# Kernel tuning notes

Measured on AMD Instinct MI355X. Metric: run time of the kernel, lower is better.

## Reference

```python
import jax, jax.numpy as jnp
import numpy as np

DIM, HEADS, WIN, SHIFT = 384, 12, 7, 3
H, W = 56, 56
HEAD_DIM = DIM // HEADS
SCALE = HEAD_DIM ** -0.5
N = WIN * WIN


def _relative_index():
    coords = np.stack(np.meshgrid(np.arange(WIN), np.arange(WIN), indexing='ij')).reshape(2, -1)
    rel = (coords[:, :, None] - coords[:, None, :]).transpose(1, 2, 0)
    rel[:, :, 0] += WIN - 1
    rel[:, :, 1] += WIN - 1
    rel[:, :, 0] *= 2 * WIN - 1
    return rel.sum(-1)  # [N, N] int


def _attn_mask():
    img = np.zeros((H, W), dtype=np.float32)
    cnt = 0
    sls = (slice(0, -WIN), slice(-WIN, -SHIFT), slice(-SHIFT, None))
    for hs in sls:
        for ws in sls:
            img[hs, ws] = cnt
            cnt += 1
    m = img.reshape(H // WIN, WIN, W // WIN, WIN).transpose(0, 2, 1, 3).reshape(-1, N)  # [nw, N]
    diff = m[:, None, :] - m[:, :, None]  # [nw, N, N]
    return np.where(diff != 0, -10000.0, 0.0).astype(np.float32)

REL_IDX = jnp.asarray(_relative_index())
MASK = jnp.asarray(_attn_mask())  # [nw, N, N]


def _layernorm(x, w, b):
    mu = x.mean(-1, keepdims=True)
    var = ((x - mu) ** 2).mean(-1, keepdims=True)
    return (x - mu) * jax.lax.rsqrt(var + 1e-5) * w + b


def _window_partition(x):  # [B,H,W,C] -> [B*nw, N, C]
    B, _, _, C = x.shape
    x = x.reshape(B, H // WIN, WIN, W // WIN, WIN, C)
    x = x.transpose(0, 1, 3, 2, 4, 5)
    return x.reshape(-1, N, C)


def _window_reverse(w, B):  # [B*nw, N, C] -> [B,H,W,C]
    C = w.shape[-1]
    x = w.reshape(B, H // WIN, W // WIN, WIN, WIN, C)
    x = x.transpose(0, 1, 3, 2, 4, 5)
    return x.reshape(B, H, W, C)


def setup_inputs() -> dict:
    key = jax.random.key(0)
    ks = jax.random.split(key, 12)
    s = DIM ** -0.5
    return {
        'x': jax.random.normal(ks[0], (32, H * W, DIM), jnp.float32),
        'qkv_w': jax.random.normal(ks[1], (DIM, 3 * DIM), jnp.float32) * s,  # stored [in,out]
        'qkv_b': jnp.zeros((3 * DIM,), jnp.float32),
        'proj_w': jax.random.normal(ks[2], (DIM, DIM), jnp.float32) * s,
        'proj_b': jnp.zeros((DIM,), jnp.float32),
        'rel_bias': jax.random.normal(ks[3], ((2 * WIN - 1) ** 2, HEADS), jnp.float32) * 0.02,
        'norm1_w': jnp.ones((DIM,), jnp.float32),
        'norm1_b': jnp.zeros((DIM,), jnp.float32),
        'norm2_w': jnp.ones((DIM,), jnp.float32),
        'norm2_b': jnp.zeros((DIM,), jnp.float32),
        'mlp_w1': jax.random.normal(ks[4], (DIM, 4 * DIM), jnp.float32) * s,
        'mlp_b1': jnp.zeros((4 * DIM,), jnp.float32),
        'mlp_w2': jax.random.normal(ks[5], (4 * DIM, DIM), jnp.float32) * (4 * DIM) ** -0.5,
        'mlp_b2': jnp.zeros((DIM,), jnp.float32),
    }


def _forward(x, qkv_w, qkv_b, proj_w, proj_b, rel_bias, norm1_w, norm1_b,
             norm2_w, norm2_b, mlp_w1, mlp_b1, mlp_w2, mlp_b2):
    B, L, C = x.shape
    residual = x
    h = _layernorm(x, norm1_w, norm1_b).reshape(B, H, W, C)
    h = jnp.roll(h, (-SHIFT, -SHIFT), axis=(1, 2))
    wx = _window_partition(h)  # [B_, N, C]
    B_ = wx.shape[0]

    qkv = (wx @ qkv_w + qkv_b).reshape(B_, N, 3, HEADS, HEAD_DIM)
    q, k, v = qkv[:, :, 0], qkv[:, :, 1], qkv[:, :, 2]  # [B_, N, h, d]
    attn = jnp.einsum('bnhd,bmhd->bhnm', q * SCALE, k)  # [B_, h, N, N]
    rb = rel_bias[REL_IDX.reshape(-1)].reshape(N, N, HEADS).transpose(2, 0, 1)
    attn = attn + rb[None]
    nw = MASK.shape[0]
    attn = attn.reshape(B_ // nw, nw, HEADS, N, N) + MASK[None, :, None]
    attn = jax.nn.softmax(attn.reshape(B_, HEADS, N, N), axis=-1)
    out = jnp.einsum('bhnm,bmhd->bnhd', attn, v).reshape(B_, N, C)
    out = out @ proj_w + proj_b

    h = _window_reverse(out, B)
    h = jnp.roll(h, (SHIFT, SHIFT), axis=(1, 2))
    x = h.reshape(B, L, C) + residual

    m = _layernorm(x, norm2_w, norm2_b)
    m = jax.nn.gelu(m @ mlp_w1 + mlp_b1, approximate=False) @ mlp_w2 + mlp_b2
    return x + m


def reference(x, qkv_w, qkv_b, proj_w, proj_b, rel_bias, norm1_w, norm1_b,
              norm2_w, norm2_b, mlp_w1, mlp_b1, mlp_w2, mlp_b2):
    return _forward(x, qkv_w, qkv_b, proj_w, proj_b, rel_bias, norm1_w, norm1_b,
                    norm2_w, norm2_b, mlp_w1, mlp_b1, mlp_w2, mlp_b2)
```

## Files before the change

kernel.cpp:

```cpp
#include <hip/hip_runtime.h>
#include <hip/hip_bf16.h>

typedef unsigned short u16;
typedef __bf16 bf16x8 __attribute__((ext_vector_type(8)));
typedef float f32x4 __attribute__((ext_vector_type(4)));

#define HH 56
#define WW 56
#define DIM 384
#define NTOK 100352
#define NWIN 2048
#define NN 49

__device__ __forceinline__ u16 f2bf(float f) {
    __hip_bfloat16 h = __float2bfloat16(f);
    return *reinterpret_cast<u16*>(&h);
}
__device__ __forceinline__ float bf2f(u16 u) {
    union { unsigned int i; float f; } c; c.i = ((unsigned int)u) << 16; return c.f;
}

__device__ __forceinline__ float fast_gelu(float x) {
    float au = fabsf(x) * 0.70710678118654752f;
    float t = __builtin_amdgcn_rcpf(fmaf(0.3275911f, au, 1.0f));
    float p = fmaf(t, 1.061405429f, -1.453152027f);
    p = fmaf(t, p, 1.421413741f);
    p = fmaf(t, p, -0.284496736f);
    p = fmaf(t, p, 0.254829592f);
    p = p * t;
    float e = __expf(-au * au);
    float erfau = fmaf(-p, e, 1.0f);
    float erfx = __builtin_copysignf(erfau, x);
    return 0.5f * x * (1.0f + erfx);
}

#define GLD_LDS(gp, lp) __builtin_amdgcn_global_load_lds( \
    (const __attribute__((address_space(1))) void*)(gp), \
    (__attribute__((address_space(3))) void*)(lp), 16, 0, 0)

__global__ void castT(const float* __restrict__ in, u16* __restrict__ out, int K, int N) {
    int i = blockIdx.x * 256 + threadIdx.x;
    if (i < N * K) {
        int n = i / K, kk = i - n * K;
        out[i] = f2bf(in[(size_t)kk * N + n]);
    }
}

__global__ void bias_kernel(const float* __restrict__ rel_bias, float* __restrict__ Tb) {
    int ty = blockIdx.x / 12, h = blockIdx.x - ty * 12;
    for (int i = threadIdx.x; i < 4096; i += 256) {
        int q = i >> 6, kk = i & 63;
        float v;
        if (kk >= 49) v = -1e30f;
        else if (q >= 49) v = 0.f;
        else {
            int rn = q / 7, cn = q - rn * 7;
            int rm = kk / 7, cm = kk - rm * 7;
            float rb = rel_bias[((rn - rm + 6) * 13 + (cn - cm + 6)) * 12 + h];
            int h0 = (ty >> 1) ? 49 : 0;
            int w0 = (ty & 1) ? 49 : 0;
            int hn = h0 + rn, hm = h0 + rm, wn = w0 + cn, wm = w0 + cm;
            int regn = (hn < 49 ? 0 : (hn < 53 ? 1 : 2)) * 3 + (wn < 49 ? 0 : (wn < 53 ? 1 : 2));
            int regm = (hm < 49 ? 0 : (hm < 53 ? 1 : 2)) * 3 + (wm < 49 ? 0 : (wm < 53 ? 1 : 2));
            v = rb + ((regn == regm) ? 0.f : -10000.f);
        }
        Tb[(size_t)blockIdx.x * 4096 + i] = v;
    }
}

template<bool WIN_MAP>
__global__ __launch_bounds__(256) void ln_kernel(
    const float* __restrict__ x, const float* __restrict__ w, const float* __restrict__ b,
    u16* __restrict__ out)
{
    int token = blockIdx.x * 4 + (threadIdx.x >> 6);
    int lane = threadIdx.x & 63;
    const float* row = x + (size_t)token * DIM;
    float v[6]; float sum = 0.f, sq = 0.f;
#pragma unroll
    for (int j = 0; j < 3; j++) {
        float2 p = *(const float2*)(row + lane * 2 + j * 128);
        v[2*j] = p.x; v[2*j+1] = p.y;
        sum += p.x + p.y; sq += p.x * p.x + p.y * p.y;
    }
#pragma unroll
    for (int off = 32; off; off >>= 1) { sum += __shfl_xor(sum, off); sq += __shfl_xor(sq, off); }
    float mu = sum * (1.f / DIM);
    float rstd = rsqrtf(sq * (1.f / DIM) - mu * mu + 1e-5f);
    size_t obase;
    if (WIN_MAP) {
        int b_ = token / 3136, hw = token - b_ * 3136;
        int h = hw / WW, wc_ = hw - h * WW;
        int hr = h - 3; if (hr < 0) hr += HH;
        int wr = wc_ - 3; if (wr < 0) wr += WW;
        int win = b_ * 64 + (hr / 7) * 8 + (wr / 7);
        int n = (hr % 7) * 7 + (wr % 7);
        obase = ((size_t)win * NN + n) * DIM;
    } else {
        obase = (size_t)token * DIM;
    }
#pragma unroll
    for (int j = 0; j < 3; j++) {
        int c = lane * 2 + j * 128;
        float a0 = (v[2*j]   - mu) * rstd * w[c]   + b[c];
        float a1 = (v[2*j+1] - mu) * rstd * w[c+1] + b[c+1];
        unsigned int pair = (unsigned int)f2bf(a0) | ((unsigned int)f2bf(a1) << 16);
        *(unsigned int*)(out + obase + c) = pair;
    }
}

template<int EPI>
__global__ __launch_bounds__(256, 3) void gemm_kernel(
    const u16* __restrict__ A, const u16* __restrict__ Bt,
    const float* __restrict__ bias, const float* __restrict__ resid,
    void* __restrict__ outp, int N, int K, int BNT)
{
    __shared__ u16 sA[3][4096];
    __shared__ u16 sB[3][4096];
    const int tid = threadIdx.x;
    const int lane = tid & 63;
    const int wave = tid >> 6;
    const int wr = wave >> 1, wc = wave & 1;

    const int q8 = gridDim.x >> 3;
    const int wg = (blockIdx.x & 7) * q8 + (blockIdx.x >> 3);
    const int bm = wg / BNT, bn = wg - bm * BNT;

    f32x4 acc[4][4] = {};

    const int r0 = tid >> 2;
    const int sg = (tid & 3) ^ (r0 & 3) ^ ((r0 >> 2) & 3);
    const u16* Arow0 = A + (size_t)(bm * 128 + r0) * K + sg * 8;
    const u16* Arow1 = Arow0 + (size_t)64 * K;
    const u16* Brow0 = Bt + (size_t)(bn * 128 + r0) * K + sg * 8;
    const u16* Brow1 = Brow0 + (size_t)64 * K;

    const int nt = K >> 5;

#define STAGE(t, buf) do { \
        int kt_ = (t) * 32; \
        GLD_LDS(Arow0 + kt_, &sA[buf][wave * 512]); \
        GLD_LDS(Arow1 + kt_, &sA[buf][2048 + wave * 512]); \
        GLD_LDS(Brow0 + kt_, &sB[buf][wave * 512]); \
        GLD_LDS(Brow1 + kt_, &sB[buf][2048 + wave * 512]); \
    } while (0)

    STAGE(0, 0); STAGE(1, 1);

    const int l15 = lane & 15, g = lane >> 4;
    const int ssr = (g ^ (l15 & 3) ^ ((l15 >> 2) & 3)) * 8;

    int buf = 0;
    for (int t = 0; t < nt; t++) {
        if (EPI == 3) {
            __builtin_amdgcn_s_barrier();
            __builtin_amdgcn_sched_barrier(0);
            if (t + 2 < nt) {
                int nb = buf + 2; if (nb >= 3) nb -= 3;
                STAGE(t + 2, nb);
            }
            int rem = nt - 1 - t; if (rem > 2) rem = 2;
            if (rem == 2)      asm volatile("s_waitcnt vmcnt(8)" ::: "memory");
            else if (rem == 1) asm volatile("s_waitcnt vmcnt(4)" ::: "memory");
            else               asm volatile("s_waitcnt vmcnt(0)" ::: "memory");
            __builtin_amdgcn_s_barrier();
            __builtin_amdgcn_sched_barrier(0);
        } else {
            if (t + 1 < nt) asm volatile("s_waitcnt vmcnt(4)" ::: "memory");
            else            asm volatile("s_waitcnt vmcnt(0)" ::: "memory");
            __builtin_amdgcn_s_barrier();
            __builtin_amdgcn_sched_barrier(0);
            if (t + 2 < nt) {
                int nb = buf + 2; if (nb >= 3) nb -= 3;
                STAGE(t + 2, nb);
            }
        }
        bf16x8 af[4], bfr[4];
#pragma unroll
        for (int m = 0; m < 4; m++) {
            int row = wr * 64 + m * 16 + l15;
            af[m] = *(const bf16x8*)&sA[buf][row * 32 + ssr];
        }
#pragma unroll
        for (int n = 0; n < 4; n++) {
            int row = wc * 64 + n * 16 + l15;
            bfr[n] = *(const bf16x8*)&sB[buf][row * 32 + ssr];
        }
#pragma unroll
        for (int m = 0; m < 4; m++)
#pragma unroll
            for (int n = 0; n < 4; n++)
                acc[m][n] = __builtin_amdgcn_mfma_f32_16x16x32_bf16(af[m], bfr[n], acc[m][n], 0, 0, 0);
        buf = buf + 1; if (buf >= 3) buf = 0;
    }
#undef STAGE

    const int col0 = bn * 128 + wc * 64 + l15;
    float bias4[4];
#pragma unroll
    for (int nn = 0; nn < 4; nn++) bias4[nn] = bias[col0 + nn * 16];

#pragma unroll
    for (int m = 0; m < 4; m++) {
#pragma unroll
        for (int r = 0; r < 4; r++) {
            int row = bm * 128 + wr * 64 + m * 16 + (g << 2) + r;
            size_t obase;
            if (EPI == 1) {
                int win = row / NN, n = row - win * NN;
                int b_ = win >> 6, wi = win & 63;
                int hr = (wi >> 3) * 7 + n / 7;
                int wcl = (wi & 7) * 7 + n % 7;
                int hf = hr + 3; if (hf >= HH) hf -= HH;
                int wf = wcl + 3; if (wf >= WW) wf -= WW;
                obase = ((size_t)b_ * 3136 + hf * WW + wf) * DIM;
            } else {
                obase = (size_t)row * N;
            }
#pragma unroll
            for (int nn = 0; nn < 4; nn++) {
                int col = col0 + nn * 16;
                float val = acc[m][nn][r] + bias4[nn];
                if (EPI == 0) {
                    ((u16*)outp)[obase + col] = f2bf(val);
                } else if (EPI == 1) {
                    ((float*)outp)[obase + col] = val + resid[obase + col];
                } else if (EPI == 2) {
                    ((u16*)outp)[obase + col] = f2bf(fast_gelu(val));
                } else {
                    ((float*)outp)[obase + col] = val + resid[obase + col];
                }
            }
        }
    }
}

__global__ __launch_bounds__(256) void attn_kernel(
    const u16* __restrict__ qkv, const float* __restrict__ Tb,
    u16* __restrict__ attn_out)
{
    __shared__ u16 smem[4][6912];
    const int win = blockIdx.x;
    const int wave = threadIdx.x >> 6;
    const int lane = threadIdx.x & 63;
    const int head = blockIdx.y * 4 + wave;
    const int l15 = lane & 15, g = lane >> 4;

    u16* Vt = smem[wave];
    u16* P  = Vt + 2304;

    const u16* qkvw = qkv + (size_t)win * NN * 1152 + head * 32;

    {
        int m = lane;
        bool real = m < NN;
        const u16* vrow = qkvw + (size_t)(real ? m : 0) * 1152 + 768;
        int4 z = {0,0,0,0};
        int4 c0 = real ? *(const int4*)(vrow)      : z;
        int4 c1 = real ? *(const int4*)(vrow + 8)  : z;
        int4 c2 = real ? *(const int4*)(vrow + 16) : z;
        int4 c3 = real ? *(const int4*)(vrow + 24) : z;
        u16 vals[32];
        *(int4*)&vals[0]  = c0; *(int4*)&vals[8]  = c1;
        *(int4*)&vals[16] = c2; *(int4*)&vals[24] = c3;
#pragma unroll
        for (int d = 0; d < 32; d++) Vt[d * 72 + m] = vals[d];
    }

    bf16x8 kf[4], qf[4];
#pragma unroll
    for (int t = 0; t < 4; t++) {
        int row = t * 16 + l15; if (row > 48) row = 48;
        const u16* base = qkvw + (size_t)row * 1152 + g * 8;
        kf[t] = *(const bf16x8*)(base + 384);
        qf[t] = *(const bf16x8*)(base);
    }
    f32x4 s[4][4];
#pragma unroll
    for (int mt = 0; mt < 4; mt++)
#pragma unroll
        for (int nt = 0; nt < 4; nt++) {
            f32x4 zero = {};
            s[mt][nt] = __builtin_amdgcn_mfma_f32_16x16x32_bf16(kf[mt], qf[nt], zero, 0, 0, 0);
        }

    const int wi = win & 63;
    const int ty = (((wi >> 3) == 7) ? 2 : 0) + (((wi & 7) == 7) ? 1 : 0);
    const float* tbb = Tb + (((size_t)ty * 12 + head) << 12);
    const float SCALE = 0.17677669529663687f;
#pragma unroll
    for (int nt = 0; nt < 4; nt++) {
        int q = nt * 16 + l15;
        const float* trow = tbb + q * 64 + g * 4;
        f32x4 b[4];
#pragma unroll
        for (int mt = 0; mt < 4; mt++) b[mt] = *(const f32x4*)(trow + mt * 16);
        float mx = -3e38f;
#pragma unroll
        for (int mt = 0; mt < 4; mt++)
#pragma unroll
            for (int r = 0; r < 4; r++) {
                float v = s[mt][nt][r] * SCALE + b[mt][r];
                s[mt][nt][r] = v;
                mx = fmaxf(mx, v);
            }
        mx = fmaxf(mx, __shfl_xor(mx, 16));
        mx = fmaxf(mx, __shfl_xor(mx, 32));
        float sum = 0.f;
#pragma unroll
        for (int mt = 0; mt < 4; mt++)
#pragma unroll
            for (int r = 0; r < 4; r++) {
                float e = __expf(s[mt][nt][r] - mx);
                s[mt][nt][r] = e;
                sum += e;
            }
        sum += __shfl_xor(sum, 16);
        sum += __shfl_xor(sum, 32);
        float inv = 1.f / sum;
#pragma unroll
        for (int mt = 0; mt < 4; mt++) {
            unsigned int p01 = (unsigned int)f2bf(s[mt][nt][0] * inv) | ((unsigned int)f2bf(s[mt][nt][1] * inv) << 16);
            unsigned int p23 = (unsigned int)f2bf(s[mt][nt][2] * inv) | ((unsigned int)f2bf(s[mt][nt][3] * inv) << 16);
            uint2 pk; pk.x = p01; pk.y = p23;
            *(uint2*)&P[(unsigned)q * 72 + mt * 16 + g * 4] = pk;
        }
    }

    bf16x8 vf[2][2];
#pragma unroll
    for (int ks = 0; ks < 2; ks++)
#pragma unroll
        for (int dt = 0; dt < 2; dt++)
            vf[ks][dt] = *(const bf16x8*)&Vt[(dt * 16 + l15) * 72 + ks * 32 + g * 8];

    f32x4 o[4][2] = {};
#pragma unroll
    for (int nt = 0; nt < 4; nt++) {
        bf16x8 pf0 = *(const bf16x8*)&P[(nt * 16 + l15) * 72 + g * 8];
        bf16x8 pf1 = *(const bf16x8*)&P[(nt * 16 + l15) * 72 + 32 + g * 8];
#pragma unroll
        for (int dt = 0; dt < 2; dt++) {
            o[nt][dt] = __builtin_amdgcn_mfma_f32_16x16x32_bf16(pf0, vf[0][dt], o[nt][dt], 0, 0, 0);
            o[nt][dt] = __builtin_amdgcn_mfma_f32_16x16x32_bf16(pf1, vf[1][dt], o[nt][dt], 0, 0, 0);
        }
    }

#pragma unroll
    for (int nt = 0; nt < 4; nt++)
#pragma unroll
        for (int r = 0; r < 4; r++) {
            int q = nt * 16 + 4 * g + r;
            if (q < NN) {
                size_t ob = ((size_t)win * NN + q) * DIM + head * 32;
                attn_out[ob + l15]      = f2bf(o[nt][0][r]);
                attn_out[ob + 16 + l15] = f2bf(o[nt][1][r]);
            }
        }
}

extern "C" void kernel_launch(void* const* d_in, const int* in_sizes, int n_in,
                              void* d_out, int out_size, void* d_ws, size_t ws_size,
                              hipStream_t stream)
{
    const float* x      = (const float*)d_in[0];
    const float* qkv_w  = (const float*)d_in[1];
    const float* qkv_b  = (const float*)d_in[2];
    const float* proj_w = (const float*)d_in[3];
    const float* proj_b = (const float*)d_in[4];
    const float* rel_b  = (const float*)d_in[5];
    const float* n1w    = (const float*)d_in[6];
    const float* n1b    = (const float*)d_in[7];
    const float* n2w    = (const float*)d_in[8];
    const float* n2b    = (const float*)d_in[9];
    const float* w1     = (const float*)d_in[10];
    const float* b1     = (const float*)d_in[11];
    const float* w2     = (const float*)d_in[12];
    const float* b2     = (const float*)d_in[13];

    char* ws = (char*)d_ws;
    u16* hidden  = (u16*)(ws);
    u16* qkvbuf  = hidden;
    float* Tb    = (float*)(ws + 231211008);
    u16* wxbuf   = (u16*)(ws + 308281344);
    u16* qkv_wt  = (u16*)(ws + 385351680);
    u16* proj_wt = (u16*)(ws + 386236416);
    u16* w1t     = (u16*)(ws + 386531328);
    u16* w2t     = (u16*)(ws + 387710976);

    castT<<<(1152*384 + 255) / 256, 256, 0, stream>>>(qkv_w, qkv_wt, 384, 1152);
    castT<<<(384*384  + 255) / 256, 256, 0, stream>>>(proj_w, proj_wt, 384, 384);
    castT<<<(384*1536 + 255) / 256, 256, 0, stream>>>(w1, w1t, 384, 1536);
    castT<<<(1536*384 + 255) / 256, 256, 0, stream>>>(w2, w2t, 1536, 384);
    bias_kernel<<<48, 256, 0, stream>>>(rel_b, Tb);

    ln_kernel<true><<<NTOK / 4, 256, 0, stream>>>(x, n1w, n1b, wxbuf);
    gemm_kernel<0><<<784 * 9, 256, 0, stream>>>(wxbuf, qkv_wt, qkv_b, nullptr, qkvbuf, 1152, 384, 9);
    attn_kernel<<<dim3(NWIN, 3), 256, 0, stream>>>(qkvbuf, Tb, wxbuf);
    gemm_kernel<1><<<784 * 3, 256, 0, stream>>>(wxbuf, proj_wt, proj_b, x, d_out, 384, 384, 3);
    ln_kernel<false><<<NTOK / 4, 256, 0, stream>>>((const float*)d_out, n2w, n2b, wxbuf);
    gemm_kernel<2><<<784 * 12, 256, 0, stream>>>(wxbuf, w1t, b1, nullptr, hidden, 1536, 384, 12);
    gemm_kernel<3><<<784 * 3, 256, 0, stream>>>(hidden, w2t, b2, (const float*)d_out, d_out, 384, 1536, 3);
}
```

Before: 929.4 us.

## Fuse window attention, output projection, residual and LayerNorm2 into one kernel

The attention kernel now handles all 12 heads of a window in one block. It keeps the per-head outputs in a swizzled LDS tile, runs the 384x384 projection GEMM directly from LDS, adds bias and the residual, writes y1, and computes LayerNorm2 statistics through LDS atomics before writing the bf16 normalized output. This removes the separate proj GEMM launch, the standalone LN2 kernel, and the round trips of the attention output and y1 through global memory. In exchange, each block uses about 80 KB of LDS, which lowers occupancy. The projection weight fragments are read straight from global memory with no LDS staging, and the special wait schedule for the EPI==3 GEMM variant is removed.

New measurement: 991.4 us. 1.07x slower.

```diff
diff --git a/kernel.cpp b/kernel.cpp
--- a/kernel.cpp
+++ b/kernel.cpp
@@ -68,7 +68,6 @@
     }
 }
 
-template<bool WIN_MAP>
 __global__ __launch_bounds__(256) void ln_kernel(
     const float* __restrict__ x, const float* __restrict__ w, const float* __restrict__ b,
     u16* __restrict__ out)
@@ -87,18 +86,13 @@
     for (int off = 32; off; off >>= 1) { sum += __shfl_xor(sum, off); sq += __shfl_xor(sq, off); }
     float mu = sum * (1.f / DIM);
     float rstd = rsqrtf(sq * (1.f / DIM) - mu * mu + 1e-5f);
-    size_t obase;
-    if (WIN_MAP) {
-        int b_ = token / 3136, hw = token - b_ * 3136;
-        int h = hw / WW, wc_ = hw - h * WW;
-        int hr = h - 3; if (hr < 0) hr += HH;
-        int wr = wc_ - 3; if (wr < 0) wr += WW;
-        int win = b_ * 64 + (hr / 7) * 8 + (wr / 7);
-        int n = (hr % 7) * 7 + (wr % 7);
-        obase = ((size_t)win * NN + n) * DIM;
-    } else {
-        obase = (size_t)token * DIM;
-    }
+    int b_ = token / 3136, hw = token - b_ * 3136;
+    int h = hw / WW, wc_ = hw - h * WW;
+    int hr = h - 3; if (hr < 0) hr += HH;
+    int wr = wc_ - 3; if (wr < 0) wr += WW;
+    int win = b_ * 64 + (hr / 7) * 8 + (wr / 7);
+    int n = (hr % 7) * 7 + (wr % 7);
+    size_t obase = ((size_t)win * NN + n) * DIM;
 #pragma unroll
     for (int j = 0; j < 3; j++) {
         int c = lane * 2 + j * 128;
@@ -152,28 +146,13 @@
 
     int buf = 0;
     for (int t = 0; t < nt; t++) {
-        if (EPI == 3) {
-            __builtin_amdgcn_s_barrier();
-            __builtin_amdgcn_sched_barrier(0);
-            if (t + 2 < nt) {
-                int nb = buf + 2; if (nb >= 3) nb -= 3;
-                STAGE(t + 2, nb);
-            }
-            int rem = nt - 1 - t; if (rem > 2) rem = 2;
-            if (rem == 2)      asm volatile("s_waitcnt vmcnt(8)" ::: "memory");
-            else if (rem == 1) asm volatile("s_waitcnt vmcnt(4)" ::: "memory");
-            else               asm volatile("s_waitcnt vmcnt(0)" ::: "memory");
-            __builtin_amdgcn_s_barrier();
-            __builtin_amdgcn_sched_barrier(0);
-        } else {
-            if (t + 1 < nt) asm volatile("s_waitcnt vmcnt(4)" ::: "memory");
-            else            asm volatile("s_waitcnt vmcnt(0)" ::: "memory");
-            __builtin_amdgcn_s_barrier();
-            __builtin_amdgcn_sched_barrier(0);
-            if (t + 2 < nt) {
-                int nb = buf + 2; if (nb >= 3) nb -= 3;
-                STAGE(t + 2, nb);
-            }
+        if (t + 1 < nt) asm volatile("s_waitcnt vmcnt(4)" ::: "memory");
+        else            asm volatile("s_waitcnt vmcnt(0)" ::: "memory");
+        __builtin_amdgcn_s_barrier();
+        __builtin_amdgcn_sched_barrier(0);
+        if (t + 2 < nt) {
+            int nb = buf + 2; if (nb >= 3) nb -= 3;
+            STAGE(t + 2, nb);
         }
         bf16x8 af[4], bfr[4];
 #pragma unroll
@@ -205,26 +184,13 @@
 #pragma unroll
         for (int r = 0; r < 4; r++) {
             int row = bm * 128 + wr * 64 + m * 16 + (g << 2) + r;
-            size_t obase;
-            if (EPI == 1) {
-                int win = row / NN, n = row - win * NN;
-                int b_ = win >> 6, wi = win & 63;
-                int hr = (wi >> 3) * 7 + n / 7;
-                int wcl = (wi & 7) * 7 + n % 7;
-                int hf = hr + 3; if (hf >= HH) hf -= HH;
-                int wf = wcl + 3; if (wf >= WW) wf -= WW;
-                obase = ((size_t)b_ * 3136 + hf * WW + wf) * DIM;
-            } else {
-                obase = (size_t)row * N;
-            }
+            size_t obase = (size_t)row * N;
 #pragma unroll
             for (int nn = 0; nn < 4; nn++) {
                 int col = col0 + nn * 16;
                 float val = acc[m][nn][r] + bias4[nn];
                 if (EPI == 0) {
                     ((u16*)outp)[obase + col] = f2bf(val);
-                } else if (EPI == 1) {
-                    ((float*)outp)[obase + col] = val + resid[obase + col];
                 } else if (EPI == 2) {
                     ((u16*)outp)[obase + col] = f2bf(fast_gelu(val));
                 } else {
@@ -235,128 +201,236 @@
     }
 }
 
-__global__ __launch_bounds__(256) void attn_kernel(
+__global__ __launch_bounds__(256) void attn_proj_kernel(
     const u16* __restrict__ qkv, const float* __restrict__ Tb,
-    u16* __restrict__ attn_out)
+    const u16* __restrict__ projw, const float* __restrict__ projb,
+    const float* __restrict__ x, const float* __restrict__ n2w,
+    const float* __restrict__ n2b, float* __restrict__ y1,
+    u16* __restrict__ ln2out)
 {
-    __shared__ u16 smem[4][6912];
+    __shared__ u16 scratch[4][6912];
+    __shared__ u16 outT[12 * 2048];
+    __shared__ float stats[64][2];
     const int win = blockIdx.x;
-    const int wave = threadIdx.x >> 6;
-    const int lane = threadIdx.x & 63;
-    const int head = blockIdx.y * 4 + wave;
+    const int tid = threadIdx.x;
+    const int wave = tid >> 6;
+    const int lane = tid & 63;
     const int l15 = lane & 15, g = lane >> 4;
 
-    u16* Vt = smem[wave];
+    u16* Vt = scratch[wave];
     u16* P  = Vt + 2304;
-
-    const u16* qkvw = qkv + (size_t)win * NN * 1152 + head * 32;
-
-    {
-        int m = lane;
-        bool real = m < NN;
-        const u16* vrow = qkvw + (size_t)(real ? m : 0) * 1152 + 768;
-        int4 z = {0,0,0,0};
-        int4 c0 = real ? *(const int4*)(vrow)      : z;
-        int4 c1 = real ? *(const int4*)(vrow + 8)  : z;
-        int4 c2 = real ? *(const int4*)(vrow + 16) : z;
-        int4 c3 = real ? *(const int4*)(vrow + 24) : z;
-        u16 vals[32];
-        *(int4*)&vals[0]  = c0; *(int4*)&vals[8]  = c1;
-        *(int4*)&vals[16] = c2; *(int4*)&vals[24] = c3;
-#pragma unroll
-        for (int d = 0; d < 32; d++) Vt[d * 72 + m] = vals[d];
-    }
-
-    bf16x8 kf[4], qf[4];
-#pragma unroll
-    for (int t = 0; t < 4; t++) {
-        int row = t * 16 + l15; if (row > 48) row = 48;
-        const u16* base = qkvw + (size_t)row * 1152 + g * 8;
-        kf[t] = *(const bf16x8*)(base + 384);
-        qf[t] = *(const bf16x8*)(base);
-    }
-    f32x4 s[4][4];
-#pragma unroll
-    for (int mt = 0; mt < 4; mt++)
-#pragma unroll
-        for (int nt = 0; nt < 4; nt++) {
-            f32x4 zero = {};
-            s[mt][nt] = __builtin_amdgcn_mfma_f32_16x16x32_bf16(kf[mt], qf[nt], zero, 0, 0, 0);
-        }
 
     const int wi = win & 63;
     const int ty = (((wi >> 3) == 7) ? 2 : 0) + (((wi & 7) == 7) ? 1 : 0);
-    const float* tbb = Tb + (((size_t)ty * 12 + head) << 12);
     const float SCALE = 0.17677669529663687f;
-#pragma unroll
-    for (int nt = 0; nt < 4; nt++) {
-        int q = nt * 16 + l15;
-        const float* trow = tbb + q * 64 + g * 4;
-        f32x4 b[4];
-#pragma unroll
-        for (int mt = 0; mt < 4; mt++) b[mt] = *(const f32x4*)(trow + mt * 16);
-        float mx = -3e38f;
+
+    for (int hi = 0; hi < 3; hi++) {
+        const int head = wave + hi * 4;
+        const u16* qkvw = qkv + (size_t)win * NN * 1152 + head * 32;
+
+        {
+            int m = lane;
+            bool real = m < NN;
+            const u16* vrow = qkvw + (size_t)(real ? m : 0) * 1152 + 768;
+            int4 z = {0,0,0,0};
+            int4 c0 = real ? *(const int4*)(vrow)      : z;
+            int4 c1 = real ? *(const int4*)(vrow + 8)  : z;
+            int4 c2 = real ? *(const int4*)(vrow + 16) : z;
+            int4 c3 = real ? *(const int4*)(vrow + 24) : z;
+            u16 vals[32];
+            *(int4*)&vals[0]  = c0; *(int4*)&vals[8]  = c1;
+            *(int4*)&vals[16] = c2; *(int4*)&vals[24] = c3;
+#pragma unroll
+            for (int d = 0; d < 32; d++) Vt[d * 72 + m] = vals[d];
+        }
+
+        bf16x8 kf[4], qf[4];
+#pragma unroll
+        for (int t = 0; t < 4; t++) {
+            int row = t * 16 + l15; if (row > 48) row = 48;
+            const u16* base = qkvw + (size_t)row * 1152 + g * 8;
+            kf[t] = *(const bf16x8*)(base + 384);
+            qf[t] = *(const bf16x8*)(base);
+        }
+        f32x4 s[4][4];
 #pragma unroll
         for (int mt = 0; mt < 4; mt++)
 #pragma unroll
-            for (int r = 0; r < 4; r++) {
-                float v = s[mt][nt][r] * SCALE + b[mt][r];
-                s[mt][nt][r] = v;
-                mx = fmaxf(mx, v);
-            }
-        mx = fmaxf(mx, __shfl_xor(mx, 16));
-        mx = fmaxf(mx, __shfl_xor(mx, 32));
-        float sum = 0.f;
-#pragma unroll
-        for (int mt = 0; mt < 4; mt++)
-#pragma unroll
-            for (int r = 0; r < 4; r++) {
-                float e = __expf(s[mt][nt][r] - mx);
-                s[mt][nt][r] = e;
-                sum += e;
-            }
-        sum += __shfl_xor(sum, 16);
-        sum += __shfl_xor(sum, 32);
-        float inv = 1.f / sum;
-#pragma unroll
-        for (int mt = 0; mt < 4; mt++) {
-            unsigned int p01 = (unsigned int)f2bf(s[mt][nt][0] * inv) | ((unsigned int)f2bf(s[mt][nt][1] * inv) << 16);
-            unsigned int p23 = (unsigned int)f2bf(s[mt][nt][2] * inv) | ((unsigned int)f2bf(s[mt][nt][3] * inv) << 16);
-            uint2 pk; pk.x = p01; pk.y = p23;
-            *(uint2*)&P[(unsigned)q * 72 + mt * 16 + g * 4] = pk;
-        }
-    }
-
-    bf16x8 vf[2][2];
-#pragma unroll
-    for (int ks = 0; ks < 2; ks++)
-#pragma unroll
-        for (int dt = 0; dt < 2; dt++)
-            vf[ks][dt] = *(const bf16x8*)&Vt[(dt * 16 + l15) * 72 + ks * 32 + g * 8];
-
-    f32x4 o[4][2] = {};
-#pragma unroll
-    for (int nt = 0; nt < 4; nt++) {
-        bf16x8 pf0 = *(const bf16x8*)&P[(nt * 16 + l15) * 72 + g * 8];
-        bf16x8 pf1 = *(const bf16x8*)&P[(nt * 16 + l15) * 72 + 32 + g * 8];
-#pragma unroll
-        for (int dt = 0; dt < 2; dt++) {
-            o[nt][dt] = __builtin_amdgcn_mfma_f32_16x16x32_bf16(pf0, vf[0][dt], o[nt][dt], 0, 0, 0);
-            o[nt][dt] = __builtin_amdgcn_mfma_f32_16x16x32_bf16(pf1, vf[1][dt], o[nt][dt], 0, 0, 0);
-        }
-    }
-
-#pragma unroll
-    for (int nt = 0; nt < 4; nt++)
+            for (int nt = 0; nt < 4; nt++) {
+                f32x4 zero = {};
+                s[mt][nt] = __builtin_amdgcn_mfma_f32_16x16x32_bf16(kf[mt], qf[nt], zero, 0, 0, 0);
+            }
+
+        const float* tbb = Tb + (((size_t)ty * 12 + head) << 12);
+#pragma unroll
+        for (int nt = 0; nt < 4; nt++) {
+            int q = nt * 16 + l15;
+            const float* trow = tbb + q * 64 + g * 4;
+            f32x4 b[4];
+#pragma unroll
+            for (int mt = 0; mt < 4; mt++) b[mt] = *(const f32x4*)(trow + mt * 16);
+            float mx = -3e38f;
+#pragma unroll
+            for (int mt = 0; mt < 4; mt++)
+#pragma unroll
+                for (int r = 0; r < 4; r++) {
+                    float v = s[mt][nt][r] * SCALE + b[mt][r];
+                    s[mt][nt][r] = v;
+                    mx = fmaxf(mx, v);
+                }
+            mx = fmaxf(mx, __shfl_xor(mx, 16));
+            mx = fmaxf(mx, __shfl_xor(mx, 32));
+            float sum = 0.f;
+#pragma unroll
+            for (int mt = 0; mt < 4; mt++)
+#pragma unroll
+                for (int r = 0; r < 4; r++) {
+                    float e = __expf(s[mt][nt][r] - mx);
+                    s[mt][nt][r] = e;
+                    sum += e;
+                }
+            sum += __shfl_xor(sum, 16);
+            sum += __shfl_xor(sum, 32);
+            float inv = 1.f / sum;
+#pragma unroll
+            for (int mt = 0; mt < 4; mt++) {
+                unsigned int p01 = (unsigned int)f2bf(s[mt][nt][0] * inv) | ((unsigned int)f2bf(s[mt][nt][1] * inv) << 16);
+                unsigned int p23 = (unsigned int)f2bf(s[mt][nt][2] * inv) | ((unsigned int)f2bf(s[mt][nt][3] * inv) << 16);
+                uint2 pk; pk.x = p01; pk.y = p23;
+                *(uint2*)&P[(unsigned)q * 72 + mt * 16 + g * 4] = pk;
+            }
+        }
+
+        bf16x8 vf[2][2];
+#pragma unroll
+        for (int ks = 0; ks < 2; ks++)
+#pragma unroll
+            for (int dt = 0; dt < 2; dt++)
+                vf[ks][dt] = *(const bf16x8*)&Vt[(dt * 16 + l15) * 72 + ks * 32 + g * 8];
+
+        f32x4 o[4][2] = {};
+#pragma unroll
+        for (int nt = 0; nt < 4; nt++) {
+            bf16x8 pf0 = *(const bf16x8*)&P[(nt * 16 + l15) * 72 + g * 8];
+            bf16x8 pf1 = *(const bf16x8*)&P[(nt * 16 + l15) * 72 + 32 + g * 8];
+#pragma unroll
+            for (int dt = 0; dt < 2; dt++) {
+                o[nt][dt] = __builtin_amdgcn_mfma_f32_16x16x32_bf16(pf0, vf[0][dt], o[nt][dt], 0, 0, 0);
+                o[nt][dt] = __builtin_amdgcn_mfma_f32_16x16x32_bf16(pf1, vf[1][dt], o[nt][dt], 0, 0, 0);
+            }
+        }
+
+        {
+            const int sw =  0; (void)sw;
+            u16* tile = &outT[head * 2048];
+#pragma unroll
+            for (int nt = 0; nt < 4; nt++)
+#pragma unroll
+                for (int r = 0; r < 4; r++) {
+                    int q = nt * 16 + 4 * g + r;
+                    int sx = r ^ g;
+                    int s0 = (l15 >> 3) ^ sx;
+                    int s1 = (2 + (l15 >> 3)) ^ sx;
+                    tile[q * 32 + s0 * 8 + (l15 & 7)] = f2bf(o[nt][0][r]);
+                    tile[q * 32 + s1 * 8 + (l15 & 7)] = f2bf(o[nt][1][r]);
+                }
+        }
+    }
+
+    if (tid < 64) { stats[tid][0] = 0.f; stats[tid][1] = 0.f; }
+    __syncthreads();
+
+    f32x4 acc[4][6] = {};
+    const int ssr = (g ^ (l15 & 3) ^ ((l15 >> 2) & 3)) * 8;
+    const int colw = wave * 96;
+#pragma unroll
+    for (int kt = 0; kt < 12; kt++) {
+        bf16x8 af[4];
+#pragma unroll
+        for (int m = 0; m < 4; m++)
+            af[m] = *(const bf16x8*)&outT[kt * 2048 + (m * 16 + l15) * 32 + ssr];
+        bf16x8 bfr[6];
+#pragma unroll
+        for (int n = 0; n < 6; n++)
+            bfr[n] = *(const bf16x8*)&projw[(size_t)(colw + n * 16 + l15) * 384 + kt * 32 + g * 8];
+#pragma unroll
+        for (int m = 0; m < 4; m++)
+#pragma unroll
+            for (int n = 0; n < 6; n++)
+                acc[m][n] = __builtin_amdgcn_mfma_f32_16x16x32_bf16(af[m], bfr[n], acc[m][n], 0, 0, 0);
+    }
+
+    float pb[6];
+#pragma unroll
+    for (int n = 0; n < 6; n++) pb[n] = projb[colw + n * 16 + l15];
+
+    const int b_ = win >> 6;
+#pragma unroll
+    for (int m = 0; m < 4; m++) {
 #pragma unroll
         for (int r = 0; r < 4; r++) {
-            int q = nt * 16 + 4 * g + r;
-            if (q < NN) {
-                size_t ob = ((size_t)win * NN + q) * DIM + head * 32;
-                attn_out[ob + l15]      = f2bf(o[nt][0][r]);
-                attn_out[ob + 16 + l15] = f2bf(o[nt][1][r]);
-            }
-        }
+            int q = m * 16 + 4 * g + r;
+            bool valid = q < NN;
+            size_t obase = 0;
+            if (valid) {
+                int hr = (wi >> 3) * 7 + q / 7;
+                int wcl = (wi & 7) * 7 + q % 7;
+                int hf = hr + 3; if (hf >= HH) hf -= HH;
+                int wf = wcl + 3; if (wf >= WW) wf -= WW;
+                obase = ((size_t)b_ * 3136 + hf * WW + wf) * DIM;
+            }
+            float s1 = 0.f, s2 = 0.f;
+#pragma unroll
+            for (int n = 0; n < 6; n++) {
+                float v = acc[m][n][r] + pb[n];
+                if (valid) {
+                    int col = colw + n * 16 + l15;
+                    v += x[obase + col];
+                    y1[obase + col] = v;
+                }
+                acc[m][n][r] = v;
+                s1 += v; s2 += v * v;
+            }
+#pragma unroll
+            for (int off = 1; off < 16; off <<= 1) {
+                s1 += __shfl_xor(s1, off);
+                s2 += __shfl_xor(s2, off);
+            }
+            if (l15 == 0) {
+                atomicAdd(&stats[q][0], s1);
+                atomicAdd(&stats[q][1], s2);
+            }
+        }
+    }
+    __syncthreads();
+
+    float w6[6], b6[6];
+#pragma unroll
+    for (int n = 0; n < 6; n++) {
+        w6[n] = n2w[colw + n * 16 + l15];
+        b6[n] = n2b[colw + n * 16 + l15];
+    }
+#pragma unroll
+    for (int m = 0; m < 4; m++) {
+#pragma unroll
+        for (int r = 0; r < 4; r++) {
+            int q = m * 16 + 4 * g + r;
+            if (q >= NN) continue;
+            int hr = (wi >> 3) * 7 + q / 7;
+            int wcl = (wi & 7) * 7 + q % 7;
+            int hf = hr + 3; if (hf >= HH) hf -= HH;
+            int wf = wcl + 3; if (wf >= WW) wf -= WW;
+            size_t obase = ((size_t)b_ * 3136 + hf * WW + wf) * DIM;
+            float mu = stats[q][0] * (1.f / DIM);
+            float rstd = rsqrtf(stats[q][1] * (1.f / DIM) - mu * mu + 1e-5f);
+#pragma unroll
+            for (int n = 0; n < 6; n++) {
+                int col = colw + n * 16 + l15;
+                float v = (acc[m][n][r] - mu) * rstd * w6[n] + b6[n];
+                ln2out[obase + col] = f2bf(v);
+            }
+        }
+    }
 }
 
 extern "C" void kernel_launch(void* const* d_in, const int* in_sizes, int n_in,
@@ -394,11 +468,10 @@
     castT<<<(1536*384 + 255) / 256, 256, 0, stream>>>(w2, w2t, 1536, 384);
     bias_kernel<<<48, 256, 0, stream>>>(rel_b, Tb);
 
-    ln_kernel<true><<<NTOK / 4, 256, 0, stream>>>(x, n1w, n1b, wxbuf);
+    ln_kernel<<<NTOK / 4, 256, 0, stream>>>(x, n1w, n1b, wxbuf);
     gemm_kernel<0><<<784 * 9, 256, 0, stream>>>(wxbuf, qkv_wt, qkv_b, nullptr, qkvbuf, 1152, 384, 9);
-    attn_kernel<<<dim3(NWIN, 3), 256, 0, stream>>>(qkvbuf, Tb, wxbuf);
-    gemm_kernel<1><<<784 * 3, 256, 0, stream>>>(wxbuf, proj_wt, proj_b, x, d_out, 384, 384, 3);
-    ln_kernel<false><<<NTOK / 4, 256, 0, stream>>>((const float*)d_out, n2w, n2b, wxbuf);
+    attn_proj_kernel<<<NWIN, 256, 0, stream>>>(qkvbuf, Tb, proj_wt, proj_b, x,
+                                               n2w, n2b, (float*)d_out, wxbuf);
     gemm_kernel<2><<<784 * 12, 256, 0, stream>>>(wxbuf, w1t, b1, nullptr, hidden, 1536, 384, 12);
     gemm_kernel<3><<<784 * 3, 256, 0, stream>>>(hidden, w2t, b2, (const float*)d_out, d_out, 384, 1536, 3);
 }
```
